# Kernel tuning notes

Hardware: AMD Instinct MI355X
Metric: run time of the kernel (lower is better)

## Reference

```python
import jax, jax.numpy as jnp
import numpy as np

EPS = 1e-5
HEADS = 4
DQK = 128
DV = 128
SCALE = DQK ** -0.5


def _bn(x, g, b, m, v):
    # inference-mode BatchNorm over channel dim (axis=1)
    inv = g / jnp.sqrt(v + EPS)
    return x * inv[None, :, None, None] + (b - m * inv)[None, :, None, None]


def setup_inputs() -> dict:
    key = jax.random.key(0)
    ks = jax.random.split(key, 16)
    f = lambda i, shape, s=1.0: jax.random.normal(ks[i], shape, dtype=jnp.float32) * s
    N, Cin, H, W = 16, 2048, 32, 32
    mid = HEADS * DV  # 512
    return {
        "x": f(0, (N, Cin, H, W)),
        "conv1_w": f(1, (mid, Cin), 0.02),
        "gamma1": 1.0 + f(2, (mid,), 0.02),
        "beta1": f(3, (mid,), 0.02),
        "mean1": f(4, (mid,), 0.02),
        "var1": 1.0 + 0.1 * jax.random.uniform(ks[5], (mid,), dtype=jnp.float32),
        "qk_w": f(6, (2 * HEADS * DQK, mid), 0.02),
        "v_w": f(7, (HEADS * DV, mid), 0.02),
        "pos_h": f(8, (H, DQK), SCALE),
        "pos_w": f(9, (W, DQK), SCALE),
        "conv3_w": f(10, (Cin, mid), 0.02),
        "gamma3": 1.0 + f(11, (Cin,), 0.02),
        "beta3": f(12, (Cin,), 0.02),
        "mean3": f(13, (Cin,), 0.02),
        "var3": 1.0 + 0.1 * jax.random.uniform(ks[14], (Cin,), dtype=jnp.float32),
    }


def reference(x, conv1_w, gamma1, beta1, mean1, var1, qk_w, v_w, pos_h, pos_w,
              conv3_w, gamma3, beta3, mean3, var3):
    n, c, h, w = x.shape
    # conv1 (1x1) + BN + ReLU
    out = jnp.einsum('nchw,oc->nohw', x, conv1_w)
    out = jax.nn.relu(_bn(out, gamma1, beta1, mean1, var1))
    # MHSA
    qk = jnp.einsum('nchw,oc->nohw', out, qk_w)  # [n, 2*heads*dqk, h, w]
    vv = jnp.einsum('nchw,oc->nohw', out, v_w)   # [n, heads*dv, h, w]
    q, k = jnp.split(qk, 2, axis=1)

    def to_heads(t):
        d = t.shape[1] // HEADS
        return t.reshape(n, HEADS, d, h * w).transpose(0, 1, 3, 2)  # [n, H, hw, d]

    q, k, vv = to_heads(q), to_heads(k), to_heads(vv)
    q = q * SCALE
    # absolute positional embedding: emb[(h w), d]
    emb = (pos_h[:, None, :] + pos_w[None, :, :]).reshape(h * w, DQK)
    logits = jnp.einsum('nhxd,nhyd->nhxy', q, k) + jnp.einsum('nhxd,yd->nhxy', q, emb)
    weights = jax.nn.softmax(logits, axis=-1)
    attn = jnp.einsum('nhxy,nhyd->nhxd', weights, vv)  # [n, H, hw, dv]
    attn = attn.transpose(0, 1, 3, 2).reshape(n, HEADS * DV, h, w)
    # stride=1 -> avg_pool is identity
    attn = jax.nn.relu(attn)
    # conv3 (1x1) + BN
    out = jnp.einsum('nchw,oc->nohw', attn, conv3_w)
    out = _bn(out, gamma3, beta3, mean3, var3)
    # residual (downsample=None, in==out channels, stride=1) + ReLU
    return jax.nn.relu(out + x)
```

## Files before the change

kernel.cpp:

```cpp
#include <hip/hip_runtime.h>
#include <stdint.h>

typedef __bf16 bf16_t;
typedef __bf16 bf16x8 __attribute__((ext_vector_type(8)));
typedef float f32x4 __attribute__((ext_vector_type(4)));

#define EPSV 1e-5f
#define QSCALE 0.08838834764831845f
#define NB 16
#define HWD 1024
#define CIN 2048
#define MID 512
#define QKVC 1536

__device__ __forceinline__ void gl_lds16(const bf16_t* g, void* l) {
    __builtin_amdgcn_global_load_lds(
        (const __attribute__((address_space(1))) uint32_t*)g,
        (__attribute__((address_space(3))) uint32_t*)l, 16, 0, 0);
}

__device__ __forceinline__ f32x4 mfma16(bf16x8 a, bf16x8 b, f32x4 c) {
    return __builtin_amdgcn_mfma_f32_16x16x32_bf16(a, b, c, 0, 0, 0);
}

#define PT1 (512*2048)
#define PT2 (PT1 + 1536*512)
#define PT3 (PT2 + 2048*512)
#define PT4 (PT3 + 1024*128)

__global__ void prep_kernel(const float* __restrict__ conv1_w,
                            const float* __restrict__ qk_w,
                            const float* __restrict__ v_w,
                            const float* __restrict__ pos_h,
                            const float* __restrict__ pos_w,
                            const float* __restrict__ conv3_w,
                            bf16_t* __restrict__ w1b, bf16_t* __restrict__ wqkvb,
                            bf16_t* __restrict__ w3b, float* __restrict__ emb) {
    int stride = gridDim.x * blockDim.x;
    for (int i = blockIdx.x * blockDim.x + threadIdx.x; i < PT4; i += stride) {
        if (i < PT1) {
            w1b[i] = (bf16_t)conv1_w[i];
        } else if (i < PT2) {
            int j = i - PT1;
            int row = j >> 9;
            float v;
            if (row < 512) v = qk_w[j] * QSCALE;
            else if (row < 1024) v = qk_w[j];
            else v = v_w[j - 512*1024];
            wqkvb[j] = (bf16_t)v;
        } else if (i < PT3) {
            int j = i - PT2;
            w3b[j] = (bf16_t)conv3_w[j];
        } else {
            int j = i - PT3;
            int y = j >> 7, d = j & 127;
            emb[j] = pos_h[(y >> 5) * 128 + d] + pos_w[(y & 31) * 128 + d];
        }
    }
}

__global__ void transpose_x_kernel(const float* __restrict__ x, bf16_t* __restrict__ xt) {
    __shared__ uint32_t tileT[64][20];
    const int n = blockIdx.z;
    const int c0 = blockIdx.x * 32;
    const int hw0 = blockIdx.y * 64;
    const int t = threadIdx.x;

    const int cp = t >> 4;
    const int hw4 = (t & 15) * 4;
    const float* p0 = x + ((size_t)n * CIN + c0 + 2 * cp) * HWD + hw0 + hw4;
    const float4 a = *(const float4*)p0;
    const float4 b = *(const float4*)(p0 + HWD);
    float av[4] = {a.x, a.y, a.z, a.w};
    float bv[4] = {b.x, b.y, b.z, b.w};
#pragma unroll
    for (int i = 0; i < 4; ++i) {
        uint16_t lo = __builtin_bit_cast(uint16_t, (bf16_t)av[i]);
        uint16_t hi = __builtin_bit_cast(uint16_t, (bf16_t)bv[i]);
        tileT[hw4 + i][cp] = (uint32_t)lo | ((uint32_t)hi << 16);
    }
    __syncthreads();
    const int hw = t >> 2;
    const int seg = (t & 3) * 4;
    uint4 v = *(const uint4*)&tileT[hw][seg];
    *(uint4*)(xt + ((size_t)n * HWD + hw0 + hw) * CIN + c0 + 2 * seg) = v;
}

__global__ void transpose_v_kernel(const bf16_t* __restrict__ qkv, bf16_t* __restrict__ vt) {
    __shared__ bf16_t tile[32][72];
    const int nh = blockIdx.z;
    const int n = nh >> 2, h = nh & 3;
    const int dv0 = blockIdx.y * 32;
    const int hw0 = blockIdx.x * 64;
    const int t = threadIdx.x;

    const int hw = t >> 2;
    const int ds = (t & 3) * 8;
    bf16x8 v = *(const bf16x8*)(qkv + ((size_t)n * HWD + hw0 + hw) * QKVC
                                + 1024 + h * 128 + dv0 + ds);
#pragma unroll
    for (int j = 0; j < 8; ++j) tile[ds + j][hw] = v[j];
    __syncthreads();
    const int dv = t >> 3;
    const int hs = (t & 7) * 8;
    uint4 o = *(const uint4*)&tile[dv][hs];
    *(uint4*)(vt + ((size_t)nh * 128 + dv0 + dv) * HWD + hw0 + hs) = o;
}

template <int EPI>
__global__ __launch_bounds__(256, 2)
void gemm_bt(const bf16_t* __restrict__ A, long long aStride,
             const bf16_t* __restrict__ B, long long bStride,
             int M, int N, int K,
             const float* __restrict__ e0, const float* __restrict__ e1,
             const float* __restrict__ e2, const float* __restrict__ e3,
             const float* __restrict__ e4, long long e4Stride,
             void* __restrict__ C, long long cStride) {
    __shared__ bf16_t As[128 * 32];
    __shared__ bf16_t Bs[128 * 32];
    const int lane = threadIdx.x & 63;
    const int wave = threadIdx.x >> 6;
    const int tN = blockIdx.x * 128, tM = blockIdx.y * 128;
    const int b = blockIdx.z;
    A += (size_t)b * aStride;
    B += (size_t)b * bStride;

    const int wm = (wave >> 1) * 64, wn = (wave & 1) * 64;
    const int lrow = lane & 15, quad = lane >> 4;
    const int sr = lane >> 2;
    const int sk = (lane & 3) * 8;

    f32x4 acc[4][4];
    const f32x4 z4 = {0.f, 0.f, 0.f, 0.f};
#pragma unroll
    for (int i = 0; i < 4; ++i)
#pragma unroll
        for (int j = 0; j < 4; ++j) acc[i][j] = z4;

    for (int k0 = 0; k0 < K; k0 += 32) {
        __syncthreads();
#pragma unroll
        for (int j = 0; j < 2; ++j) {
            const int g = wave * 2 + j;
            const int row = g * 16 + sr;
            gl_lds16(A + (size_t)(tM + row) * K + k0 + sk, (char*)As + g * 1024 + lane * 16);
            gl_lds16(B + (size_t)(tN + row) * K + k0 + sk, (char*)Bs + g * 1024 + lane * 16);
        }
        __syncthreads();
        bf16x8 af[4], bfr[4];
#pragma unroll
        for (int t = 0; t < 4; ++t) {
            af[t]  = *(const bf16x8*)(As + (wm + t * 16 + lrow) * 32 + quad * 8);
            bfr[t] = *(const bf16x8*)(Bs + (wn + t * 16 + lrow) * 32 + quad * 8);
        }
#pragma unroll
        for (int i = 0; i < 4; ++i)
#pragma unroll
            for (int j = 0; j < 4; ++j)
                acc[i][j] = mfma16(af[i], bfr[j], acc[i][j]);
    }

#pragma unroll
    for (int i = 0; i < 4; ++i) {
        const int row0 = tM + wm + i * 16 + quad * 4;
        float inv3[4], bb3[4];
        if constexpr (EPI == 3) {
#pragma unroll
            for (int r = 0; r < 4; ++r) {
                float g = e0[row0 + r], be = e1[row0 + r], mn = e2[row0 + r], vr = e3[row0 + r];
                float inv = g * rsqrtf(vr + EPSV);
                inv3[r] = inv;
                bb3[r] = be - mn * inv;
            }
        }
#pragma unroll
        for (int j = 0; j < 4; ++j) {
            const int col = tN + wn + j * 16 + lrow;
            if constexpr (EPI == 1) {
                float g = e0[col], be = e1[col], mn = e2[col], vr = e3[col];
                float inv = g * rsqrtf(vr + EPSV);
                float bb = be - mn * inv;
                bf16_t* Cb = (bf16_t*)C + (size_t)b * cStride;
#pragma unroll
                for (int r = 0; r < 4; ++r) {
                    float v = fmaxf(acc[i][j][r] * inv + bb, 0.f);
                    Cb[(size_t)(row0 + r) * MID + col] = (bf16_t)v;
                }
            } else if constexpr (EPI == 2) {
                bf16_t* Cb = (bf16_t*)C + (size_t)b * cStride;
                const bool addEmb = (col >= 512) && (col < 1024);
#pragma unroll
                for (int r = 0; r < 4; ++r) {
                    float v = acc[i][j][r];
                    if (addEmb) v += e4[(size_t)(row0 + r) * 128 + (col & 127)];
                    Cb[(size_t)(row0 + r) * QKVC + col] = (bf16_t)v;
                }
            } else {
                float* Cf = (float*)C + (size_t)b * cStride;
                const float* xr = e4 + (size_t)b * e4Stride;
#pragma unroll
                for (int r = 0; r < 4; ++r) {
                    float v = acc[i][j][r] * inv3[r] + bb3[r] + xr[(size_t)(row0 + r) * HWD + col];
                    Cf[(size_t)(row0 + r) * HWD + col] = fmaxf(v, 0.f);
                }
            }
        }
    }
}

__global__ __launch_bounds__(256, 2)
void attn_kernel(const bf16_t* __restrict__ qkv, const bf16_t* __restrict__ vt,
                 bf16_t* __restrict__ attn) {
    __shared__ bf16_t Ks[64 * 128];
    __shared__ bf16_t Vs[128 * 64];
    __shared__ bf16_t Ps[4 * 32 * 64];
    const int lane = threadIdx.x & 63;
    const int wave = threadIdx.x >> 6;
    const int qb = blockIdx.x, h = blockIdx.y, n = blockIdx.z;
    const int lrow = lane & 15, quad = lane >> 4;
    const int q0 = qb * 128 + wave * 32;

    bf16x8 qf[2][4];
#pragma unroll
    for (int rt = 0; rt < 2; ++rt)
#pragma unroll
        for (int kf = 0; kf < 4; ++kf)
            qf[rt][kf] = *(const bf16x8*)(qkv + (size_t)(n * HWD + q0 + rt * 16 + lrow) * QKVC
                                          + h * 128 + kf * 32 + quad * 8);

    f32x4 o[2][8];
    const f32x4 z4 = {0.f, 0.f, 0.f, 0.f};
#pragma unroll
    for (int rt = 0; rt < 2; ++rt)
#pragma unroll
        for (int d = 0; d < 8; ++d) o[rt][d] = z4;
    float l[2][4];
#pragma unroll
    for (int rt = 0; rt < 2; ++rt)
#pragma unroll
        for (int r = 0; r < 4; ++r) l[rt][r] = 0.f;

    const bf16_t* kbase = qkv + (size_t)n * HWD * QKVC + 512 + h * 128;
    const bf16_t* vbase = vt + (size_t)((n * 4 + h) * 128) * HWD;

    for (int kc = 0; kc < 16; ++kc) {
        __syncthreads();
#pragma unroll
        for (int j = 0; j < 4; ++j) {
            const int g = wave * 4 + j;
            const int krow = g * 4 + quad;
            const int kgl = lrow ^ (krow & 15);
            gl_lds16(kbase + (size_t)(kc * 64 + krow) * QKVC + kgl * 8,
                     (char*)Ks + g * 1024 + lane * 16);
            const int vrow = g * 8 + (lane >> 3);
            const int vgl = (lane & 7) ^ (vrow & 7);
            gl_lds16(vbase + (size_t)vrow * HWD + kc * 64 + vgl * 8,
                     (char*)Vs + g * 1024 + lane * 16);
        }
        __syncthreads();

        f32x4 s[2][4];
#pragma unroll
        for (int rt = 0; rt < 2; ++rt)
#pragma unroll
            for (int ct = 0; ct < 4; ++ct) s[rt][ct] = z4;
#pragma unroll
        for (int kf = 0; kf < 4; ++kf) {
#pragma unroll
            for (int ct = 0; ct < 4; ++ct) {
                bf16x8 kfrag = *(const bf16x8*)(Ks + (ct * 16 + lrow) * 128
                                                + ((kf * 4 + quad) ^ lrow) * 8);
                s[0][ct] = mfma16(qf[0][kf], kfrag, s[0][ct]);
                s[1][ct] = mfma16(qf[1][kf], kfrag, s[1][ct]);
            }
        }

#pragma unroll
        for (int rt = 0; rt < 2; ++rt) {
#pragma unroll
            for (int r = 0; r < 4; ++r) {
                const int prow = rt * 16 + quad * 4 + r;
                float rs = 0.f;
#pragma unroll
                for (int ct = 0; ct < 4; ++ct) {
                    float p = __expf(s[rt][ct][r]);
                    rs += p;
                    const int pg = (ct * 2 + (lrow >> 3)) ^ (prow & 7);
                    Ps[wave * 2048 + prow * 64 + pg * 8 + (lrow & 7)] = (bf16_t)p;
                }
                l[rt][r] += rs;
            }
        }
        asm volatile("s_waitcnt lgkmcnt(0)" ::: "memory");

#pragma unroll
        for (int kf = 0; kf < 2; ++kf) {
            bf16x8 pa0 = *(const bf16x8*)(Ps + wave * 2048 + lrow * 64
                                          + ((kf * 4 + quad) ^ (lrow & 7)) * 8);
            bf16x8 pa1 = *(const bf16x8*)(Ps + wave * 2048 + (16 + lrow) * 64
                                          + ((kf * 4 + quad) ^ (lrow & 7)) * 8);
#pragma unroll
            for (int d = 0; d < 8; ++d) {
                bf16x8 vf = *(const bf16x8*)(Vs + (d * 16 + lrow) * 64
                                             + ((kf * 4 + quad) ^ (lrow & 7)) * 8);
                o[0][d] = mfma16(pa0, vf, o[0][d]);
                o[1][d] = mfma16(pa1, vf, o[1][d]);
            }
        }
    }

#pragma unroll
    for (int rt = 0; rt < 2; ++rt)
#pragma unroll
        for (int r = 0; r < 4; ++r) {
#pragma unroll
            for (int off = 1; off < 16; off <<= 1)
                l[rt][r] += __shfl_xor(l[rt][r], off, 64);
        }

#pragma unroll
    for (int rt = 0; rt < 2; ++rt) {
#pragma unroll
        for (int r = 0; r < 4; ++r) {
            float linv = 1.f / l[rt][r];
            const size_t row = (size_t)n * HWD + q0 + rt * 16 + quad * 4 + r;
#pragma unroll
            for (int d = 0; d < 8; ++d) {
                float v = o[rt][d][r] * linv;
                v = fmaxf(v, 0.f);
                attn[row * MID + h * 128 + d * 16 + lrow] = (bf16_t)v;
            }
        }
    }
}

extern "C" void kernel_launch(void* const* d_in, const int* in_sizes, int n_in,
                              void* d_out, int out_size, void* d_ws, size_t ws_size,
                              hipStream_t stream) {
    const float* x       = (const float*)d_in[0];
    const float* conv1_w = (const float*)d_in[1];
    const float* gamma1  = (const float*)d_in[2];
    const float* beta1   = (const float*)d_in[3];
    const float* mean1   = (const float*)d_in[4];
    const float* var1    = (const float*)d_in[5];
    const float* qk_w    = (const float*)d_in[6];
    const float* v_w     = (const float*)d_in[7];
    const float* pos_h   = (const float*)d_in[8];
    const float* pos_w   = (const float*)d_in[9];
    const float* conv3_w = (const float*)d_in[10];
    const float* gamma3  = (const float*)d_in[11];
    const float* beta3   = (const float*)d_in[12];
    const float* mean3   = (const float*)d_in[13];
    const float* var3    = (const float*)d_in[14];
    float* out = (float*)d_out;

    char* ws = (char*)d_ws;
    size_t off = 0;
    auto carve = [&](size_t bytes) {
        void* p = ws + off;
        off += (bytes + 255) & ~(size_t)255;
        return p;
    };
    bf16_t* Xt    = (bf16_t*)carve((size_t)NB * HWD * CIN * 2);
    bf16_t* C1t   = (bf16_t*)carve((size_t)NB * HWD * MID * 2);
    bf16_t* QKVt  = (bf16_t*)carve((size_t)NB * HWD * QKVC * 2);
    bf16_t* Vt    = (bf16_t*)carve((size_t)NB * 512 * HWD * 2);
    bf16_t* AttnT = (bf16_t*)carve((size_t)NB * HWD * MID * 2);
    bf16_t* W1b   = (bf16_t*)carve((size_t)512 * 2048 * 2);
    bf16_t* Wqkvb = (bf16_t*)carve((size_t)1536 * 512 * 2);
    bf16_t* W3b   = (bf16_t*)carve((size_t)2048 * 512 * 2);
    float*  Emb   = (float*)carve((size_t)1024 * 128 * 4);

    prep_kernel<<<2048, 256, 0, stream>>>(conv1_w, qk_w, v_w, pos_h, pos_w, conv3_w,
                                          W1b, Wqkvb, W3b, Emb);

    transpose_x_kernel<<<dim3(64, 16, NB), 256, 0, stream>>>(x, Xt);

    gemm_bt<1><<<dim3(4, 8, NB), 256, 0, stream>>>(
        Xt, (long long)HWD * CIN, W1b, 0, HWD, MID, CIN,
        gamma1, beta1, mean1, var1, nullptr, 0, C1t, (long long)HWD * MID);

    gemm_bt<2><<<dim3(12, 8, NB), 256, 0, stream>>>(
        C1t, (long long)HWD * MID, Wqkvb, 0, HWD, QKVC, MID,
        nullptr, nullptr, nullptr, nullptr, Emb, 0, QKVt, (long long)HWD * QKVC);

    transpose_v_kernel<<<dim3(16, 4, NB * 4), 256, 0, stream>>>(QKVt, Vt);

    attn_kernel<<<dim3(8, 4, NB), 256, 0, stream>>>(QKVt, Vt, AttnT);

    gemm_bt<3><<<dim3(8, 16, NB), 256, 0, stream>>>(
        W3b, 0, AttnT, (long long)HWD * MID, CIN, HWD, MID,
        gamma3, beta3, mean3, var3, x, (long long)CIN * HWD, out, (long long)CIN * HWD);
}
```

Measured before the change: 513.8 us.

## Compute V directly transposed via separate GEMM, widen GEMM K-tile with XOR swizzle

Splits the fused QKV projection into a QK GEMM and a separate V GEMM that treats the weight as A and activations as B, so V comes out already in [dv, hw] layout. This removes the standalone V transpose kernel and its extra global round trip. The generic GEMM now stages a 64-wide K slice into LDS with an XOR swizzle to avoid bank conflicts, halves the number of barrier pairs, and raises launch bounds to 3 blocks per CU. The larger LDS tiles (32KB per block) and higher occupancy target may press on registers.

```diff
diff --git a/kernel.cpp b/kernel.cpp
--- a/kernel.cpp
+++ b/kernel.cpp
@@ -11,7 +11,7 @@
 #define HWD 1024
 #define CIN 2048
 #define MID 512
-#define QKVC 1536
+#define QKLD 1024
 
 __device__ __forceinline__ void gl_lds16(const bf16_t* g, void* l) {
     __builtin_amdgcn_global_load_lds(
@@ -23,10 +23,11 @@
     return __builtin_amdgcn_mfma_f32_16x16x32_bf16(a, b, c, 0, 0, 0);
 }
 
-#define PT1 (512*2048)
-#define PT2 (PT1 + 1536*512)
-#define PT3 (PT2 + 2048*512)
-#define PT4 (PT3 + 1024*128)
+#define PW1 (512*2048)
+#define PQK (PW1 + 1024*512)
+#define PV  (PQK + 512*512)
+#define PW3 (PV  + 2048*512)
+#define PE  (PW3 + 1024*128)
 
 __global__ void prep_kernel(const float* __restrict__ conv1_w,
                             const float* __restrict__ qk_w,
@@ -34,25 +35,26 @@
                             const float* __restrict__ pos_h,
                             const float* __restrict__ pos_w,
                             const float* __restrict__ conv3_w,
-                            bf16_t* __restrict__ w1b, bf16_t* __restrict__ wqkvb,
-                            bf16_t* __restrict__ w3b, float* __restrict__ emb) {
+                            bf16_t* __restrict__ w1b, bf16_t* __restrict__ wqkb,
+                            bf16_t* __restrict__ wvb, bf16_t* __restrict__ w3b,
+                            float* __restrict__ emb) {
     int stride = gridDim.x * blockDim.x;
-    for (int i = blockIdx.x * blockDim.x + threadIdx.x; i < PT4; i += stride) {
-        if (i < PT1) {
+    for (int i = blockIdx.x * blockDim.x + threadIdx.x; i < PE; i += stride) {
+        if (i < PW1) {
             w1b[i] = (bf16_t)conv1_w[i];
-        } else if (i < PT2) {
-            int j = i - PT1;
+        } else if (i < PQK) {
+            int j = i - PW1;
             int row = j >> 9;
-            float v;
-            if (row < 512) v = qk_w[j] * QSCALE;
-            else if (row < 1024) v = qk_w[j];
-            else v = v_w[j - 512*1024];
-            wqkvb[j] = (bf16_t)v;
-        } else if (i < PT3) {
-            int j = i - PT2;
+            float v = (row < 512) ? qk_w[j] * QSCALE : qk_w[j];
+            wqkb[j] = (bf16_t)v;
+        } else if (i < PV) {
+            int j = i - PQK;
+            wvb[j] = (bf16_t)v_w[j];
+        } else if (i < PW3) {
+            int j = i - PV;
             w3b[j] = (bf16_t)conv3_w[j];
         } else {
-            int j = i - PT3;
+            int j = i - PW3;
             int y = j >> 7, d = j & 127;
             emb[j] = pos_h[(y >> 5) * 128 + d] + pos_w[(y & 31) * 128 + d];
         }
@@ -86,38 +88,17 @@
     *(uint4*)(xt + ((size_t)n * HWD + hw0 + hw) * CIN + c0 + 2 * seg) = v;
 }
 
-__global__ void transpose_v_kernel(const bf16_t* __restrict__ qkv, bf16_t* __restrict__ vt) {
-    __shared__ bf16_t tile[32][72];
-    const int nh = blockIdx.z;
-    const int n = nh >> 2, h = nh & 3;
-    const int dv0 = blockIdx.y * 32;
-    const int hw0 = blockIdx.x * 64;
-    const int t = threadIdx.x;
-
-    const int hw = t >> 2;
-    const int ds = (t & 3) * 8;
-    bf16x8 v = *(const bf16x8*)(qkv + ((size_t)n * HWD + hw0 + hw) * QKVC
-                                + 1024 + h * 128 + dv0 + ds);
-#pragma unroll
-    for (int j = 0; j < 8; ++j) tile[ds + j][hw] = v[j];
-    __syncthreads();
-    const int dv = t >> 3;
-    const int hs = (t & 7) * 8;
-    uint4 o = *(const uint4*)&tile[dv][hs];
-    *(uint4*)(vt + ((size_t)nh * 128 + dv0 + dv) * HWD + hw0 + hs) = o;
-}
-
 template <int EPI>
-__global__ __launch_bounds__(256, 2)
+__global__ __launch_bounds__(256, 3)
 void gemm_bt(const bf16_t* __restrict__ A, long long aStride,
              const bf16_t* __restrict__ B, long long bStride,
-             int M, int N, int K,
+             int K, int ldc,
              const float* __restrict__ e0, const float* __restrict__ e1,
              const float* __restrict__ e2, const float* __restrict__ e3,
              const float* __restrict__ e4, long long e4Stride,
              void* __restrict__ C, long long cStride) {
-    __shared__ bf16_t As[128 * 32];
-    __shared__ bf16_t Bs[128 * 32];
+    __shared__ bf16_t As[128 * 64];
+    __shared__ bf16_t Bs[128 * 64];
     const int lane = threadIdx.x & 63;
     const int wave = threadIdx.x >> 6;
     const int tN = blockIdx.x * 128, tM = blockIdx.y * 128;
@@ -127,8 +108,9 @@
 
     const int wm = (wave >> 1) * 64, wn = (wave & 1) * 64;
     const int lrow = lane & 15, quad = lane >> 4;
-    const int sr = lane >> 2;
-    const int sk = (lane & 3) * 8;
+    const int srow = lane >> 3;
+    const int sgr = lane & 7;
+    const int lg = sgr ^ srow;
 
     f32x4 acc[4][4];
     const f32x4 z4 = {0.f, 0.f, 0.f, 0.f};
@@ -137,27 +119,34 @@
 #pragma unroll
         for (int j = 0; j < 4; ++j) acc[i][j] = z4;
 
-    for (int k0 = 0; k0 < K; k0 += 32) {
+    for (int k0 = 0; k0 < K; k0 += 64) {
         __syncthreads();
 #pragma unroll
-        for (int j = 0; j < 2; ++j) {
-            const int g = wave * 2 + j;
-            const int row = g * 16 + sr;
-            gl_lds16(A + (size_t)(tM + row) * K + k0 + sk, (char*)As + g * 1024 + lane * 16);
-            gl_lds16(B + (size_t)(tN + row) * K + k0 + sk, (char*)Bs + g * 1024 + lane * 16);
+        for (int j = 0; j < 4; ++j) {
+            const int blk = wave * 4 + j;
+            const int row = blk * 8 + srow;
+            gl_lds16(A + (size_t)(tM + row) * K + k0 + lg * 8,
+                     (char*)As + blk * 1024 + lane * 16);
+            gl_lds16(B + (size_t)(tN + row) * K + k0 + lg * 8,
+                     (char*)Bs + blk * 1024 + lane * 16);
         }
         __syncthreads();
-        bf16x8 af[4], bfr[4];
-#pragma unroll
-        for (int t = 0; t < 4; ++t) {
-            af[t]  = *(const bf16x8*)(As + (wm + t * 16 + lrow) * 32 + quad * 8);
-            bfr[t] = *(const bf16x8*)(Bs + (wn + t * 16 + lrow) * 32 + quad * 8);
-        }
-#pragma unroll
-        for (int i = 0; i < 4; ++i)
-#pragma unroll
-            for (int j = 0; j < 4; ++j)
-                acc[i][j] = mfma16(af[i], bfr[j], acc[i][j]);
+#pragma unroll
+        for (int kh = 0; kh < 2; ++kh) {
+            bf16x8 af[4], bfr[4];
+#pragma unroll
+            for (int t = 0; t < 4; ++t) {
+                const int ar = wm + t * 16 + lrow;
+                af[t] = *(const bf16x8*)(As + ar * 64 + (((kh * 4 + quad) ^ (ar & 7)) * 8));
+                const int br = wn + t * 16 + lrow;
+                bfr[t] = *(const bf16x8*)(Bs + br * 64 + (((kh * 4 + quad) ^ (br & 7)) * 8));
+            }
+#pragma unroll
+            for (int i = 0; i < 4; ++i)
+#pragma unroll
+                for (int j = 0; j < 4; ++j)
+                    acc[i][j] = mfma16(af[i], bfr[j], acc[i][j]);
+        }
     }
 
 #pragma unroll
@@ -184,24 +173,29 @@
 #pragma unroll
                 for (int r = 0; r < 4; ++r) {
                     float v = fmaxf(acc[i][j][r] * inv + bb, 0.f);
-                    Cb[(size_t)(row0 + r) * MID + col] = (bf16_t)v;
+                    Cb[(size_t)(row0 + r) * ldc + col] = (bf16_t)v;
                 }
             } else if constexpr (EPI == 2) {
                 bf16_t* Cb = (bf16_t*)C + (size_t)b * cStride;
-                const bool addEmb = (col >= 512) && (col < 1024);
+                const bool addEmb = (col >= 512);
 #pragma unroll
                 for (int r = 0; r < 4; ++r) {
                     float v = acc[i][j][r];
                     if (addEmb) v += e4[(size_t)(row0 + r) * 128 + (col & 127)];
-                    Cb[(size_t)(row0 + r) * QKVC + col] = (bf16_t)v;
+                    Cb[(size_t)(row0 + r) * ldc + col] = (bf16_t)v;
                 }
+            } else if constexpr (EPI == 4) {
+                bf16_t* Cb = (bf16_t*)C + (size_t)b * cStride;
+#pragma unroll
+                for (int r = 0; r < 4; ++r)
+                    Cb[(size_t)(row0 + r) * ldc + col] = (bf16_t)acc[i][j][r];
             } else {
                 float* Cf = (float*)C + (size_t)b * cStride;
                 const float* xr = e4 + (size_t)b * e4Stride;
 #pragma unroll
                 for (int r = 0; r < 4; ++r) {
-                    float v = acc[i][j][r] * inv3[r] + bb3[r] + xr[(size_t)(row0 + r) * HWD + col];
-                    Cf[(size_t)(row0 + r) * HWD + col] = fmaxf(v, 0.f);
+                    float v = acc[i][j][r] * inv3[r] + bb3[r] + xr[(size_t)(row0 + r) * ldc + col];
+                    Cf[(size_t)(row0 + r) * ldc + col] = fmaxf(v, 0.f);
                 }
             }
         }
@@ -209,7 +203,7 @@
 }
 
 __global__ __launch_bounds__(256, 2)
-void attn_kernel(const bf16_t* __restrict__ qkv, const bf16_t* __restrict__ vt,
+void attn_kernel(const bf16_t* __restrict__ qkt, const bf16_t* __restrict__ vt,
                  bf16_t* __restrict__ attn) {
     __shared__ bf16_t Ks[64 * 128];
     __shared__ bf16_t Vs[128 * 64];
@@ -225,7 +219,7 @@
     for (int rt = 0; rt < 2; ++rt)
 #pragma unroll
         for (int kf = 0; kf < 4; ++kf)
-            qf[rt][kf] = *(const bf16x8*)(qkv + (size_t)(n * HWD + q0 + rt * 16 + lrow) * QKVC
+            qf[rt][kf] = *(const bf16x8*)(qkt + (size_t)(n * HWD + q0 + rt * 16 + lrow) * QKLD
                                           + h * 128 + kf * 32 + quad * 8);
 
     f32x4 o[2][8];
@@ -240,7 +234,7 @@
 #pragma unroll
         for (int r = 0; r < 4; ++r) l[rt][r] = 0.f;
 
-    const bf16_t* kbase = qkv + (size_t)n * HWD * QKVC + 512 + h * 128;
+    const bf16_t* kbase = qkt + (size_t)n * HWD * QKLD + 512 + h * 128;
     const bf16_t* vbase = vt + (size_t)((n * 4 + h) * 128) * HWD;
 
     for (int kc = 0; kc < 16; ++kc) {
@@ -250,7 +244,7 @@
             const int g = wave * 4 + j;
             const int krow = g * 4 + quad;
             const int kgl = lrow ^ (krow & 15);
-            gl_lds16(kbase + (size_t)(kc * 64 + krow) * QKVC + kgl * 8,
+            gl_lds16(kbase + (size_t)(kc * 64 + krow) * QKLD + kgl * 8,
                      (char*)Ks + g * 1024 + lane * 16);
             const int vrow = g * 8 + (lane >> 3);
             const int vgl = (lane & 7) ^ (vrow & 7);
@@ -363,32 +357,35 @@
     };
     bf16_t* Xt    = (bf16_t*)carve((size_t)NB * HWD * CIN * 2);
     bf16_t* C1t   = (bf16_t*)carve((size_t)NB * HWD * MID * 2);
-    bf16_t* QKVt  = (bf16_t*)carve((size_t)NB * HWD * QKVC * 2);
+    bf16_t* QKt   = (bf16_t*)carve((size_t)NB * HWD * QKLD * 2);
     bf16_t* Vt    = (bf16_t*)carve((size_t)NB * 512 * HWD * 2);
     bf16_t* AttnT = (bf16_t*)carve((size_t)NB * HWD * MID * 2);
     bf16_t* W1b   = (bf16_t*)carve((size_t)512 * 2048 * 2);
-    bf16_t* Wqkvb = (bf16_t*)carve((size_t)1536 * 512 * 2);
+    bf16_t* Wqkb  = (bf16_t*)carve((size_t)1024 * 512 * 2);
+    bf16_t* Wvb   = (bf16_t*)carve((size_t)512 * 512 * 2);
     bf16_t* W3b   = (bf16_t*)carve((size_t)2048 * 512 * 2);
     float*  Emb   = (float*)carve((size_t)1024 * 128 * 4);
 
     prep_kernel<<<2048, 256, 0, stream>>>(conv1_w, qk_w, v_w, pos_h, pos_w, conv3_w,
-                                          W1b, Wqkvb, W3b, Emb);
+                                          W1b, Wqkb, Wvb, W3b, Emb);
 
     transpose_x_kernel<<<dim3(64, 16, NB), 256, 0, stream>>>(x, Xt);
 
     gemm_bt<1><<<dim3(4, 8, NB), 256, 0, stream>>>(
-        Xt, (long long)HWD * CIN, W1b, 0, HWD, MID, CIN,
+        Xt, (long long)HWD * CIN, W1b, 0, CIN, MID,
         gamma1, beta1, mean1, var1, nullptr, 0, C1t, (long long)HWD * MID);
 
-    gemm_bt<2><<<dim3(12, 8, NB), 256, 0, stream>>>(
-        C1t, (long long)HWD * MID, Wqkvb, 0, HWD, QKVC, MID,
-        nullptr, nullptr, nullptr, nullptr, Emb, 0, QKVt, (long long)HWD * QKVC);
-
-    transpose_v_kernel<<<dim3(16, 4, NB * 4), 256, 0, stream>>>(QKVt, Vt);
-
-    attn_kernel<<<dim3(8, 4, NB), 256, 0, stream>>>(QKVt, Vt, AttnT);
+    gemm_bt<2><<<dim3(8, 8, NB), 256, 0, stream>>>(
+        C1t, (long long)HWD * MID, Wqkb, 0, MID, QKLD,
+        nullptr, nullptr, nullptr, nullptr, Emb, 0, QKt, (long long)HWD * QKLD);
+
+    gemm_bt<4><<<dim3(8, 4, NB), 256, 0, stream>>>(
+        Wvb, 0, C1t, (long long)HWD * MID, MID, HWD,
+        nullptr, nullptr, nullptr, nullptr, nullptr, 0, Vt, (long long)512 * HWD);
+
+    attn_kernel<<<dim3(8, 4, NB), 256, 0, stream>>>(QKt, Vt, AttnT);
 
     gemm_bt<3><<<dim3(8, 16, NB), 256, 0, stream>>>(
-        W3b, 0, AttnT, (long long)HWD * MID, CIN, HWD, MID,
+        W3b, 0, AttnT, (long long)HWD * MID, MID, HWD,
         gamma3, beta3, mean3, var3, x, (long long)CIN * HWD, out, (long long)CIN * HWD);
 }
```

Result: faster. 479.5 us (-6.7%).
